# Kernel tuning notes

Hardware: AMD Instinct MI355X
Metric: run time of the kernel (lower is better)

Reference implementation:

```python
import jax, jax.numpy as jnp
import numpy as np
from jax import lax

B = 2; H = 96; W = 96
WS = 8; SHIFT = WS // 2; NW = H // WS; P = WS * WS
NH = 3; HD = 32; CD = 96; TD = 96
MID = 2 * CD; GA = 16; BASES = 16

def _rel_index():
    g = np.stack(np.meshgrid(np.arange(WS), np.arange(WS), indexing='ij'), -1).reshape(-1, 2)
    rel = g[:, None, :] - g[None, :, :] + WS - 1
    return jnp.asarray(rel[..., 0] * (2 * WS - 1) + rel[..., 1])  # [P, P]

REL_IDX = _rel_index()

def _sw_mask():
    m = np.zeros((NW, NW, WS, WS, WS, WS), bool); s = WS - SHIFT
    m[-1, :, :s, :, s:, :] = True
    m[-1, :, s:, :, :s, :] = True
    m[:, -1, :, :s, :, s:] = True
    m[:, -1, :, s:, :, :s] = True
    return jnp.asarray(m.reshape(NW * NW, P, P))

SW_MASK = _sw_mask()

def _ln(x, g, b, eps=1e-5):
    mu = x.mean(-1, keepdims=True)
    v = ((x - mu) ** 2).mean(-1, keepdims=True)
    return (x - mu) * lax.rsqrt(v + eps) * g + b

def _conv1x1(x, w):
    return jnp.einsum('bchw,oc->bohw', x, w)

def _conv3x3(x, w, b=None, groups=1):
    y = lax.conv_general_dilated(x, w, (1, 1), ((1, 1), (1, 1)),
                                 dimension_numbers=('NCHW', 'OIHW', 'NCHW'),
                                 feature_group_count=groups)
    return y if b is None else y + b[None, :, None, None]

def _unfold3(x):
    # torch F.unfold(k=3,p=1): channel-major patch order (c, kh, kw)
    bs, c, h, w = x.shape
    xp = jnp.pad(x, ((0, 0), (0, 0), (1, 1), (1, 1)))
    pats = jnp.stack([xp[:, :, i:i + h, j:j + w] for i in range(3) for j in range(3)], axis=2)
    return pats.reshape(bs, c * 9, h * w)

def _adaconv(x, ada_w, p1w, p1b, p2w, p2b):
    bs, c, h, w = x.shape
    para = jax.nn.relu(_conv1x1(x, p1w) + p1b[None, :, None, None])
    para = _conv3x3(para, p2w, p2b).reshape(bs, BASES, h * w)      # [b, r, p]
    xu = _unfold3(x).reshape(bs, GA, (c // GA) * 9, h * w)          # [b, g, d, p]
    # out[b,g,o,p] = sum_{d,r} ada_w[g,o,d,r] * xu[b,g,d,p] * para[b,r,p]
    t = jnp.einsum('godr,bgdp->bgorp', ada_w, xu)
    out = jnp.einsum('bgorp,brp->bgop', t, para)
    return out.reshape(bs, c, h, w)

def _conv_block(x, ln_g, ln_b, c1_pw, c1_dw, c2_pw, ada_w, p1w, p1b, p2w, p2b, c3_w):
    r = _ln(x.transpose(0, 2, 3, 1), ln_g, ln_b).transpose(0, 3, 1, 2)
    b1 = _conv3x3(_conv1x1(r, c1_pw), c1_dw, groups=MID)
    b2 = jax.nn.gelu(_adaconv(_conv1x1(r, c2_pw), ada_w, p1w, p1b, p2w, p2b), approximate=False)
    return x + _conv1x1(b1 * b2, c3_w)

def _wmsa(x, qkv_w, qkv_b, rel_pos, proj_w, proj_b):
    bs = x.shape[0]
    x = jnp.roll(x, (-SHIFT, -SHIFT), (1, 2))
    qkv = jnp.einsum('bhwc,oc->bhwo', x, qkv_w) + qkv_b
    qkv = qkv.reshape(bs, NW, WS, NW, WS, 3, NH, HD)
    qkv = qkv.transpose(5, 6, 0, 1, 3, 2, 4, 7).reshape(3, NH, bs, NW * NW, P, HD)
    q, k, v = qkv[0], qkv[1], qkv[2]
    sim = jnp.einsum('hbwpc,hbwqc->hbwpq', q, k) * (HD ** -0.5)
    bias = rel_pos[REL_IDX.reshape(-1)].reshape(P, P, NH).transpose(2, 0, 1)
    sim = sim + bias[:, None, None]
    sim = jnp.where(SW_MASK[None, None], -jnp.inf, sim)
    attn = jax.nn.softmax(sim, axis=-1)
    out = jnp.einsum('hbwpq,hbwqc->hbwpc', attn, v)
    out = out.reshape(NH, bs, NW, NW, WS, WS, HD).transpose(1, 2, 4, 3, 5, 0, 6).reshape(bs, H, W, NH * HD)
    out = jnp.einsum('bhwc,oc->bhwo', out, proj_w) + proj_b
    return jnp.roll(out, (SHIFT, SHIFT), (1, 2))

def _swin_block(x, ln1_g, ln1_b, qkv_w, qkv_b, rel_pos, proj_w, proj_b,
                ln2_g, ln2_b, f_w1, f_b1, f_dw, f_db, f_w2, f_b2):
    xt = x.transpose(0, 2, 3, 1)  # b h w c
    xt = xt + _wmsa(_ln(xt, ln1_g, ln1_b), qkv_w, qkv_b, rel_pos, proj_w, proj_b)
    y = _ln(xt, ln2_g, ln2_b).transpose(0, 3, 1, 2)
    y = _conv1x1(y, f_w1) + f_b1[None, :, None, None]
    y = _conv3x3(y, f_dw, f_db, groups=2 * TD)
    y = jax.nn.gelu(y, approximate=False)
    y = _conv1x1(y, f_w2) + f_b2[None, :, None, None]
    xt = xt + y.transpose(0, 2, 3, 1)
    return xt.transpose(0, 3, 1, 2)

def _block(x, cb_ln_g, cb_ln_b, cb_c1_pw, cb_c1_dw, cb_c2_pw, ada_w, ada_p1_w, ada_p1_b,
           ada_p2_w, ada_p2_b, cb_c3_w, ln1_g, ln1_b, qkv_w, qkv_b, rel_pos, proj_w, proj_b,
           ln2_g, ln2_b, ffn_w1, ffn_b1, ffn_dw, ffn_db, ffn_w2, ffn_b2, out_w, out_b):
    conv_x, trans_x = x[:, :CD], x[:, CD:]
    conv_x = _conv_block(conv_x, cb_ln_g, cb_ln_b, cb_c1_pw, cb_c1_dw, cb_c2_pw,
                         ada_w, ada_p1_w, ada_p1_b, ada_p2_w, ada_p2_b, cb_c3_w)
    trans_x = _swin_block(trans_x, ln1_g, ln1_b, qkv_w, qkv_b, rel_pos, proj_w, proj_b,
                          ln2_g, ln2_b, ffn_w1, ffn_b1, ffn_dw, ffn_db, ffn_w2, ffn_b2)
    res = _conv1x1(jnp.concatenate([conv_x, trans_x], axis=1), out_w) + out_b[None, :, None, None]
    return x + res

def setup_inputs():
    key = jax.random.key(0)
    ks = jax.random.split(key, 20)
    n = lambda i, shape, s=0.05: jax.random.normal(ks[i], shape, jnp.float32) * s
    return {
        'x': jax.random.normal(ks[0], (B, CD + TD, H, W), jnp.float32),
        'cb_ln_g': jnp.ones((CD,), jnp.float32), 'cb_ln_b': jnp.zeros((CD,), jnp.float32),
        'cb_c1_pw': n(1, (MID, CD)), 'cb_c1_dw': n(2, (MID, 1, 3, 3)),
        'cb_c2_pw': n(3, (MID, CD)),
        'ada_w': n(4, (GA, MID // GA, (MID // GA) * 9, BASES)),
        'ada_p1_w': n(5, (BASES, MID)), 'ada_p1_b': jnp.zeros((BASES,), jnp.float32),
        'ada_p2_w': n(6, (BASES, BASES, 3, 3)), 'ada_p2_b': jnp.zeros((BASES,), jnp.float32),
        'cb_c3_w': n(7, (CD, MID)),
        'ln1_g': jnp.ones((TD,), jnp.float32), 'ln1_b': jnp.zeros((TD,), jnp.float32),
        'qkv_w': n(8, (3 * TD, TD)), 'qkv_b': jnp.zeros((3 * TD,), jnp.float32),
        'rel_pos': n(9, ((2 * WS - 1) ** 2, NH), 0.02),
        'proj_w': n(10, (TD, TD)), 'proj_b': jnp.zeros((TD,), jnp.float32),
        'ln2_g': jnp.ones((TD,), jnp.float32), 'ln2_b': jnp.zeros((TD,), jnp.float32),
        'ffn_w1': n(11, (2 * TD, TD)), 'ffn_b1': jnp.zeros((2 * TD,), jnp.float32),
        'ffn_dw': n(12, (2 * TD, 1, 3, 3)), 'ffn_db': jnp.zeros((2 * TD,), jnp.float32),
        'ffn_w2': n(13, (TD, 2 * TD)), 'ffn_b2': jnp.zeros((TD,), jnp.float32),
        'out_w': n(14, (CD + TD, CD + TD)), 'out_b': jnp.zeros((CD + TD,), jnp.float32),
    }

def reference(x, cb_ln_g, cb_ln_b, cb_c1_pw, cb_c1_dw, cb_c2_pw, ada_w, ada_p1_w, ada_p1_b,
              ada_p2_w, ada_p2_b, cb_c3_w, ln1_g, ln1_b, qkv_w, qkv_b, rel_pos, proj_w, proj_b,
              ln2_g, ln2_b, ffn_w1, ffn_b1, ffn_dw, ffn_db, ffn_w2, ffn_b2, out_w, out_b):
    return _block(x, cb_ln_g, cb_ln_b, cb_c1_pw, cb_c1_dw, cb_c2_pw, ada_w, ada_p1_w, ada_p1_b,
                  ada_p2_w, ada_p2_b, cb_c3_w, ln1_g, ln1_b, qkv_w, qkv_b, rel_pos, proj_w, proj_b,
                  ln2_g, ln2_b, ffn_w1, ffn_b1, ffn_dw, ffn_db, ffn_w2, ffn_b2, out_w, out_b)
```

## Files before the change

### kernel.cpp

```cpp
#include <hip/hip_runtime.h>
#include <math.h>

#define HW_ 9216
#define IH 96
#define IW 96
#define NB 2
#define ST (NB*HW_)

typedef __attribute__((ext_vector_type(8))) short bf16x8;
typedef __attribute__((ext_vector_type(4))) float f32x4;
typedef unsigned short u16;

__device__ __forceinline__ float gelu_f(float v){
  return 0.5f*v*(1.0f+erff(v*0.70710678118654752440f));
}
__device__ __forceinline__ unsigned f2bf(float f){
  unsigned u = __float_as_uint(f);
  return (u + 0x7FFF + ((u>>16)&1)) >> 16;
}
__device__ __forceinline__ float bfl(unsigned u){ return __uint_as_float(u<<16); }
__device__ __forceinline__ float bfh(unsigned u){ return __uint_as_float(u & 0xffff0000u); }

__device__ __forceinline__ void ln12_body(const float* __restrict__ x,
    const float* __restrict__ g1, const float* __restrict__ b1,
    const float* __restrict__ g2, const float* __restrict__ b2,
    u16* __restrict__ lnc, u16* __restrict__ ln1o,
    float* __restrict__ xc, float* __restrict__ xt, int bidx)
{
  __shared__ float t[192][33];
  const int p0 = bidx<<5;
  const int bb = p0/HW_, hw0 = p0 - bb*HW_;
  const int tid = threadIdx.x;
  const int px = tid & 31, cr = tid >> 5;
  const float* xb = x + (size_t)bb*192*HW_ + hw0;
  #pragma unroll
  for (int k=0;k<24;k++){
    int c = cr + k*8;
    t[c][px] = xb[(size_t)c*HW_ + px];
  }
  __syncthreads();
  const int lane = tid&63, wv = tid>>6;
  #pragma unroll 1
  for (int i=0;i<8;i++){
    const int lp = wv*8+i;
    const size_t p = p0 + lp;
    float a0 = t[lane][lp];
    float a1 = (lane<32)? t[64+lane][lp] : 0.f;
    float c0 = t[96+lane][lp];
    float c1 = (lane<32)? t[160+lane][lp] : 0.f;
    float s1=a0+a1, s2=c0+c1;
    #pragma unroll
    for (int o=32;o;o>>=1){ s1+=__shfl_xor(s1,o); s2+=__shfl_xor(s2,o); }
    const float mu1=s1*(1.f/96.f), mu2=s2*(1.f/96.f);
    const float d0=a0-mu1, d1=a1-mu1, e0=c0-mu2, e1=c1-mu2;
    float q1=d0*d0+((lane<32)?d1*d1:0.f), q2=e0*e0+((lane<32)?e1*e1:0.f);
    #pragma unroll
    for (int o=32;o;o>>=1){ q1+=__shfl_xor(q1,o); q2+=__shfl_xor(q2,o); }
    const float r1=rsqrtf(q1*(1.f/96.f)+1e-5f), r2=rsqrtf(q2*(1.f/96.f)+1e-5f);
    lnc [p*96+lane] = (u16)f2bf(d0*r1*g1[lane]+b1[lane]);
    ln1o[p*96+lane] = (u16)f2bf(e0*r2*g2[lane]+b2[lane]);
    xc  [p*96+lane] = a0;
    xt  [p*96+lane] = c0;
    if (lane<32){
      lnc [p*96+64+lane] = (u16)f2bf(d1*r1*g1[64+lane]+b1[64+lane]);
      ln1o[p*96+64+lane] = (u16)f2bf(e1*r2*g2[64+lane]+b2[64+lane]);
      xc  [p*96+64+lane] = a1;
      xt  [p*96+64+lane] = c1;
    }
  }
}

__device__ __forceinline__ void ln_body(const float* __restrict__ in, int istride,
    const float* __restrict__ gam, const float* __restrict__ bet,
    u16* __restrict__ out, int bidx)
{
  int lane = threadIdx.x & 63;
  int wv   = threadIdx.x >> 6;
  int p    = (bidx << 2) + wv;
  const float* row = in + (size_t)p*istride;
  float v0 = row[lane];
  float v1 = (lane < 32) ? row[64+lane] : 0.0f;
  float s = v0 + v1;
  #pragma unroll
  for (int o=32;o;o>>=1) s += __shfl_xor(s,o);
  float mu = s * (1.0f/96.0f);
  float d0 = v0 - mu;
  float d1 = v1 - mu;
  float qv = d0*d0 + ((lane<32)? d1*d1 : 0.0f);
  #pragma unroll
  for (int o=32;o;o>>=1) qv += __shfl_xor(qv,o);
  float rstd = rsqrtf(qv*(1.0f/96.0f) + 1e-5f);
  u16* orow = out + (size_t)p*96;
  orow[lane] = (u16)f2bf(d0*rstd*gam[lane] + bet[lane]);
  if (lane < 32) orow[64+lane] = (u16)f2bf(d1*rstd*gam[64+lane] + bet[64+lane]);
}

template<int ACT, bool CONCAT, bool FINAL, bool HASB, bool HASR, bool OUTBF, bool SPLIT>
__device__ __forceinline__ void conv_body(unsigned char* smem,
    const u16* __restrict__ in1, const float* __restrict__ in2f, int istride,
    const u16* __restrict__ wbf, const float* __restrict__ bias,
    const float* __restrict__ res, int rstride,
    void* __restrict__ out, int ostride, int Cin, int Cout,
    u16* __restrict__ out2, int bx, int by)
{
  unsigned char* actl = smem;
  unsigned char* wl   = smem + 26624;
  const int tid=threadIdx.x, lane=tid&63, wv=tid>>6;
  const int lr=lane&15, g4=lane>>4, wm=wv>>1, wn=wv&1;
  const int p0=bx<<7, co0=by<<6;

  f32x4 acc[2][4];
  #pragma unroll
  for (int m=0;m<2;m++)
    #pragma unroll
    for (int n=0;n<4;n++) acc[m][n]=(f32x4){0.f,0.f,0.f,0.f};

  for (int kc=0; kc<Cin; kc+=96){
    {
      const int row=tid>>1, half=tid&1;
      if (!CONCAT || kc==0){
        const u16* rp = in1 + (size_t)(p0+row)*istride + (CONCAT?0:kc) + half*48;
        #pragma unroll
        for (int s=0;s<6;s++)
          *(uint4*)(actl + row*208 + (half*6+s)*16) = *(const uint4*)(rp + s*8);
      } else {
        const float* rp = in2f + (size_t)(p0+row)*96 + half*48;
        #pragma unroll
        for (int s=0;s<6;s++){
          float4 a=*(const float4*)(rp+s*8), b=*(const float4*)(rp+s*8+4);
          uint4 pk;
          pk.x=f2bf(a.x)|(f2bf(a.y)<<16);
          pk.y=f2bf(a.z)|(f2bf(a.w)<<16);
          pk.z=f2bf(b.x)|(f2bf(b.y)<<16);
          pk.w=f2bf(b.z)|(f2bf(b.w)<<16);
          *(uint4*)(actl + row*208 + (half*6+s)*16) = pk;
        }
      }
    }
    {
      const int row=tid&63, grp=tid>>6;
      const int co=co0+row;
      const u16* wr = wbf + (size_t)co*Cin + kc;
      #pragma unroll
      for (int s=0;s<3;s++){
        int sl=grp*3+s;
        uint4 v={0,0,0,0};
        if (co<Cout) v=*(const uint4*)(wr + sl*8);
        *(uint4*)(wl + row*208 + sl*16)=v;
      }
    }
    __syncthreads();
    #pragma unroll
    for (int ks=0;ks<3;ks++){
      const int sl=ks*4+g4;
      bf16x8 afr[2], bfr[4];
      #pragma unroll
      for (int m=0;m<2;m++) afr[m]=*(const bf16x8*)(wl + ((wm*2+m)*16+lr)*208 + sl*16);
      #pragma unroll
      for (int n=0;n<4;n++) bfr[n]=*(const bf16x8*)(actl + (wn*64+n*16+lr)*208 + sl*16);
      #pragma unroll
      for (int m=0;m<2;m++)
        #pragma unroll
        for (int n=0;n<4;n++)
          acc[m][n]=__builtin_amdgcn_mfma_f32_16x16x32_bf16(afr[m], bfr[n], acc[m][n],0,0,0);
    }
    __syncthreads();
  }

  if (FINAL){
    float* outf = (float*)out;
    #pragma unroll
    for (int m=0;m<2;m++){
      const int cb=co0+(wm*2+m)*16+(g4<<2);
      float4 bv = make_float4(0.f,0.f,0.f,0.f);
      if (HASB) bv = *(const float4*)(bias+cb);
      #pragma unroll
      for (int n=0;n<4;n++){
        const int p=p0+wn*64+n*16+lr;
        const int bb=p/HW_, hw=p-bb*HW_;
        const float av[4]={acc[m][n].x,acc[m][n].y,acc[m][n].z,acc[m][n].w};
        const float bvv[4]={bv.x,bv.y,bv.z,bv.w};
        #pragma unroll
        for (int j=0;j<4;j++){
          size_t oi=((size_t)bb*192+cb+j)*HW_+hw;
          outf[oi]=av[j]+bvv[j]+res[oi];
        }
      }
    }
    return;
  }
  float* lt=(float*)smem;
  #pragma unroll
  for (int m=0;m<2;m++)
    #pragma unroll
    for (int n=0;n<4;n++){
      int px=wn*64+n*16+lr;
      int c=(wm*2+m)*16+(g4<<2);
      *(f32x4*)&lt[px*68+c]=acc[m][n];
    }
  __syncthreads();
  {
    const int pr=tid>>1, half=tid&1;
    const int p=p0+pr;
    #pragma unroll
    for (int s=0;s<8;s++){
      int cl=half*32+s*4;
      int co=co0+cl;
      if (co<Cout){
        float4 v=*(float4*)&lt[pr*68+cl];
        if (SPLIT){
          if (co>=384){
            const int c2 = co-384;
            const float4 bv=*(const float4*)(bias+c2);
            v.x=fmaxf(v.x+bv.x,0.f); v.y=fmaxf(v.y+bv.y,0.f);
            v.z=fmaxf(v.z+bv.z,0.f); v.w=fmaxf(v.w+bv.w,0.f);
            uint2 pk;
            pk.x = f2bf(v.x)|(f2bf(v.y)<<16);
            pk.y = f2bf(v.z)|(f2bf(v.w)<<16);
            *(uint2*)((u16*)out + (size_t)p*16 + c2) = pk;
          } else {
            const int cc = (co<192)? co : co-192;
            const int gg = cc/12, cll = cc - gg*12;
            u16* dst = out2 + ((co<192)? (size_t)0 : (size_t)ST*192)
                     + ((size_t)gg*ST + p)*12 + cll;
            uint2 pk;
            pk.x = f2bf(v.x)|(f2bf(v.y)<<16);
            pk.y = f2bf(v.z)|(f2bf(v.w)<<16);
            *(uint2*)dst = pk;
          }
          continue;
        }
        if (HASB){ const float4 bv=*(const float4*)(bias+co); v.x+=bv.x;v.y+=bv.y;v.z+=bv.z;v.w+=bv.w; }
        if (ACT==1){
          v.x=fmaxf(v.x,0.f); v.y=fmaxf(v.y,0.f); v.z=fmaxf(v.z,0.f); v.w=fmaxf(v.w,0.f);
        }
        if (HASR){ const float4 rv=*(const float4*)(res+(size_t)p*rstride+co); v.x+=rv.x;v.y+=rv.y;v.z+=rv.z;v.w+=rv.w; }
        if (OUTBF){
          uint2 pk;
          pk.x = f2bf(v.x)|(f2bf(v.y)<<16);
          pk.y = f2bf(v.z)|(f2bf(v.w)<<16);
          *(uint2*)((u16*)out + (size_t)p*ostride + co) = pk;
        } else {
          *(float4*)((float*)out + (size_t)p*ostride + co) = v;
        }
      }
    }
  }
}

template<int ACT, bool CONCAT, bool FINAL, bool HASB, bool HASR, bool OUTBF, bool SPLIT>
__global__ __launch_bounds__(256) void conv_mfma_k(
    const u16* __restrict__ in1, const float* __restrict__ in2f, int istride,
    const u16* __restrict__ wbf, const float* __restrict__ bias,
    const float* __restrict__ res, int rstride,
    void* __restrict__ out, int ostride, int Cin, int Cout,
    u16* __restrict__ out2)
{
  __shared__ __align__(16) unsigned char smem[39936];
  conv_body<ACT,CONCAT,FINAL,HASB,HASR,OUTBF,SPLIT>(smem, in1, in2f, istride, wbf, bias,
      res, rstride, out, ostride, Cin, Cout, out2, blockIdx.x, blockIdx.y);
}

__device__ __forceinline__ void adaconv_body(unsigned char* smem,
    const u16* __restrict__ x1g, const u16* __restrict__ x2g,
    const float* __restrict__ para, const u16* __restrict__ apre,
    const float* __restrict__ dww, u16* __restrict__ outb2,
    int b, int g, int reg)
{
  unsigned char* HB2 = smem;
  unsigned char* HB1 = smem + 8640;
  float* PS = (float*)(smem + 17280);
  float* OS = (float*)(smem + 27520);
  float* WDW = (float*)(smem + 33664);

  const int tid=threadIdx.x, lane=tid&63, wv=tid>>6;
  const int lr=lane&15, g4=lane>>4;
  const int hi=(lane>>5)&1, lo16=(lane>>4)&1;
  const int rh=(reg/12)<<4, rw=(reg%12)<<3;

  bf16x8 af[3][5];
  {
    const u16* ag = apre + (size_t)g*30720;
    #pragma unroll
    for (int oo=0;oo<3;oo++){
      const int row=(wv*3+oo)*16+lr;
      #pragma unroll
      for (int ks=0;ks<5;ks++)
        af[oo][ks] = *(const bf16x8*)(ag + row*160 + ks*32 + g4*8);
    }
  }
  if (tid < 180){
    int hy = tid/10, hx = tid - hy*10;
    int gy = rh+hy-1, gx = rw+hx-1;
    uint2 a2={0,0},b2={0,0},c2={0,0}, a1={0,0},b1={0,0},c1={0,0};
    if ((unsigned)gy<IH && (unsigned)gx<IW){
      const size_t base = ((size_t)g*ST + (size_t)b*HW_ + gy*IW + gx)*12;
      const u16* s2 = x2g + base;
      a2=*(const uint2*)s2; b2=*(const uint2*)(s2+4); c2=*(const uint2*)(s2+8);
      const u16* s1 = x1g + base;
      a1=*(const uint2*)s1; b1=*(const uint2*)(s1+4); c1=*(const uint2*)(s1+8);
    }
    *(uint4*)(HB2 + tid*48)      = make_uint4(a2.x,a2.y,b2.x,b2.y);
    *(uint4*)(HB2 + tid*48 + 16) = make_uint4(c2.x,c2.y,0,0);
    *(uint4*)(HB1 + tid*48)      = make_uint4(a1.x,a1.y,b1.x,b1.y);
    *(uint4*)(HB1 + tid*48 + 16) = make_uint4(c1.x,c1.y,0,0);
  }
  if (tid < 108) WDW[tid] = dww[g*108 + tid];
  #pragma unroll
  for (int it=0; it<2; ++it){
    int idx = tid + (it<<8);
    int sub = idx >> 8;
    int p = (idx>>2)&63, q = idx&3;
    int gy = rh + (sub<<3) + (p>>3), gx = rw + (p&7);
    float4 v = *(const float4*)(para + ((size_t)b*HW_+gy*IW+gx)*16 + q*4);
    *(float4*)&PS[sub*1280 + p*20 + q*4] = v;
  }
  __syncthreads();

  int tapoff[5];
  tapoff[0] = hi ? 48   : 0;
  tapoff[1] = hi ? 480  : 96;
  tapoff[2] = hi ? 576  : 528;
  tapoff[3] = hi ? 1008 : 960;
  tapoff[4] = 1056;

  #pragma unroll
  for (int sub=0; sub<2; ++sub){
    const int sy = sub<<3;
    const int base0 = ((sy + (lr>>3))*10 + (lr&7))*48 + lo16*16;

    f32x4 acc[3][4];
    #pragma unroll
    for (int oo=0;oo<3;oo++)
      #pragma unroll
      for (int n=0;n<4;n++) acc[oo][n]=(f32x4){0.f,0.f,0.f,0.f};

    #pragma unroll
    for (int ks=0;ks<5;ks++){
      bf16x8 bfr[4];
      #pragma unroll
      for (int n=0;n<4;n++)
        bfr[n] = *(const bf16x8*)(HB2 + base0 + n*960 + tapoff[ks]);
      #pragma unroll
      for (int oo=0;oo<3;oo++)
        #pragma unroll
        for (int n=0;n<4;n++)
          acc[oo][n]=__builtin_amdgcn_mfma_f32_16x16x32_bf16(af[oo][ks], bfr[n], acc[oo][n],0,0,0);
    }

    const float* ps = &PS[sub*1280];
    #pragma unroll
    for (int oo=0;oo<3;oo++){
      const int o=wv*3+oo;
      #pragma unroll
      for (int n=0;n<4;n++){
        const int p=(n<<4)+lr;
        const f32x4 prv = *(const f32x4*)&ps[p*20+(g4<<2)];
        float s=acc[oo][n].x*prv.x+acc[oo][n].y*prv.y+acc[oo][n].z*prv.z+acc[oo][n].w*prv.w;
        s += __shfl_xor(s,16); s += __shfl_xor(s,32);
        if (g4==n) OS[((sub<<6)+p)*12+o] = gelu_f(s);
      }
    }
  }
  __syncthreads();
  {
    const size_t gb = (size_t)b*HW_;
    for (int idx=tid; idx<384; idx+=256){
      const int cq = idx % 3;
      const int rest = idx / 3;
      const int p = rest & 63, sub = rest >> 6;
      const int py = p>>3, px = p&7;
      const int Y = (sub<<3)+py, X = px;
      const unsigned char* hb1 = HB1 + (Y*10+X)*48 + cq*8;
      const float* wd = &WDW[cq*36];
      float v0=0.f,v1=0.f,v2=0.f,v3=0.f;
      #pragma unroll
      for (int i=0;i<3;i++){
        #pragma unroll
        for (int j=0;j<3;j++){
          const uint2 r = *(const uint2*)(hb1 + (i*10+j)*48);
          const int tp=i*3+j;
          v0 += bfl(r.x)*wd[tp];      v1 += bfh(r.x)*wd[9+tp];
          v2 += bfl(r.y)*wd[18+tp];   v3 += bfh(r.y)*wd[27+tp];
        }
      }
      const size_t gi = (gb + (rh+(sub<<3)+py)*IW + (rw+px))*192 + g*12 + cq*4;
      const float* os = &OS[((sub<<6)+p)*12 + cq*4];
      uint2 pk;
      pk.x = f2bf(os[0]*v0) | (f2bf(os[1]*v1)<<16);
      pk.y = f2bf(os[2]*v2) | (f2bf(os[3]*v3)<<16);
      *(uint2*)(outb2 + gi) = pk;
    }
  }
}

__device__ __forceinline__ void allprep_body(
    const float* __restrict__ s0, const float* __restrict__ s1,
    const float* __restrict__ s2, const float* __restrict__ s3,
    const float* __restrict__ s4, const float* __restrict__ s5,
    const float* __restrict__ s6, const float* __restrict__ s7,
    const float* __restrict__ p1w, const float* __restrict__ aw,
    u16* __restrict__ wdst, u16* __restrict__ apre, int bid)
{
  const int tid = threadIdx.x;
  if (bid < 648){
    const int blks[8]={108,72,72,72,36,72,72,144};
    const int off[8] ={0,27648,46080,66048,84480,93696,112128,130560};
    const int sz[8]  ={27648,18432,18432,18432,9216,18432,18432,36864};
    int m=0, acc=0;
    #pragma unroll
    for (int k=0;k<8;k++){ if (bid >= acc + blks[k]){ acc += blks[k]; m=k+1; } }
    const float* s = (m==0)?s0:(m==1)?s1:(m==2)?s2:(m==3)?s3:(m==4)?s4:(m==5)?s5:(m==6)?s6:s7;
    int i = (bid-acc)*256 + tid;
    if (i < sz[m]) wdst[off[m]+i] = (u16)f2bf(s[i]);
  } else if (bid < 654){
    int i = (bid-648)*256 + tid;
    if (i < 1536){
      int o = i/96, ci = i - o*96;
      float s = 0.f;
      for (int k=0;k<192;k++) s += p1w[o*192+k]*s2[k*96+ci];
      wdst[64512+i] = (u16)f2bf(s);
    }
  } else {
    int E = (bid-654)*256 + tid;
    int g = E / 30720, e = E - g*30720;
    int row = e / 160, kp = e - row*160;
    int tap = kp >> 4, cl = kp & 15;
    int o = row >> 4, r = row & 15;
    float v = 0.f;
    if (tap < 9 && cl < 12)
      v = aw[(((size_t)(g*12+o)*108) + cl*9 + tap)*16 + r];
    apre[(size_t)g*30720 + e] = (u16)f2bf(v);
  }
}

__global__ __launch_bounds__(256) void prep_ln12_k(
    const float* s0, const float* s1, const float* s2, const float* s3,
    const float* s4, const float* s5, const float* s6, const float* s7,
    const float* p1w, const float* aw, u16* wdst, u16* apre,
    const float* x, const float* g1, const float* b1,
    const float* g2, const float* b2,
    u16* lnc, u16* ln1o, float* xc, float* xt)
{
  const int bid = blockIdx.x;
  if (bid < 2574)
    allprep_body(s0,s1,s2,s3,s4,s5,s6,s7,p1w,aw,wdst,apre,bid);
  else
    ln12_body(x,g1,b1,g2,b2,lnc,ln1o,xc,xt,bid-2574);
}

__global__ __launch_bounds__(256) void gemm12_k(
    const u16* lnc, const u16* r6, const u16* wc12p, const float* p1b,
    const u16* wqkv, const float* qkvb, u16* pa1, u16* x1g, u16* qkv)
{
  __shared__ __align__(16) unsigned char smem[39936];
  if (blockIdx.y < 7)
    conv_body<0,false,false,false,false,true,true>(smem, lnc, nullptr, 96, wc12p, p1b,
        nullptr, 0, pa1, 16, 96, 400, x1g, blockIdx.x, blockIdx.y);
  else
    conv_body<0,false,false,true,false,true,false>(smem, r6, nullptr, 96, wqkv, qkvb,
        nullptr, 0, qkv, 288, 96, 288, nullptr, blockIdx.x, blockIdx.y-7);
}

__global__ __launch_bounds__(256) void ada_proj_k(
    const u16* x1g, const u16* x2g, const float* para, const u16* apre,
    const float* dww, u16* outb2,
    const u16* r6, const u16* wproj, const float* projb, float* xt)
{
  __shared__ __align__(16) unsigned char smem[39936];
  const int bid = blockIdx.x;
  if (bid < 2304){
    const int b = bid / 1152, rem = bid - b*1152;
    const int g = rem / 72, reg = rem - g*72;
    adaconv_body(smem, x1g, x2g, para, apre, dww, outb2, b, g, reg);
  } else {
    const int bx = bid - 2304;
    conv_body<0,false,false,true,true,false,false>(smem, r6, nullptr, 96, wproj, projb,
        xt, 96, xt, 96, 96, 96, nullptr, bx % 144, bx / 144);
  }
}

__global__ __launch_bounds__(256) void c3_ln2_k(
    const u16* b2b, const u16* wc3, const float* xc, u16* r4,
    const float* xt, const float* g2, const float* bt2, u16* r6)
{
  __shared__ __align__(16) unsigned char smem[39936];
  const int bid = blockIdx.x;
  if (bid < 288)
    conv_body<0,false,false,false,true,true,false>(smem, b2b, nullptr, 192, wc3, nullptr,
        xc, 96, r4, 96, 192, 96, nullptr, bid % 144, bid / 144);
  else
    ln_body(xt, 96, g2, bt2, r6, bid-288);
}

template<bool HASB, bool DOGELU>
__global__ __launch_bounds__(256) void dw3x3_k(const u16* __restrict__ in, int istride,
                                               const float* __restrict__ w,
                                               const float* __restrict__ bias,
                                               u16* __restrict__ out, int C){
  int t = blockIdx.x*256 + threadIdx.x;
  int cg = C >> 2;
  int p = t / cg;
  if (p >= ST) return;
  int c4 = (t - p*cg) << 2;
  int bb = p / HW_, hw = p - bb*HW_;
  int hy = hw / IW, wx = hw - hy*IW;
  float w0[9], w1[9], w2[9], w3[9];
  #pragma unroll
  for (int tp=0;tp<9;tp++){
    w0[tp]=w[(c4+0)*9+tp]; w1[tp]=w[(c4+1)*9+tp]; w2[tp]=w[(c4+2)*9+tp]; w3[tp]=w[(c4+3)*9+tp];
  }
  float ax=0.f, ay=0.f, az=0.f, aw=0.f;
  #pragma unroll
  for (int i=0;i<3;i++){
    int y = hy+i-1;
    if ((unsigned)y >= IH) continue;
    #pragma unroll
    for (int j=0;j<3;j++){
      int x2 = wx+j-1;
      if ((unsigned)x2 >= IW) continue;
      const uint2 r = *(const uint2*)(in + ((size_t)bb*HW_ + y*IW + x2)*istride + c4);
      int tp=i*3+j;
      ax += bfl(r.x)*w0[tp]; ay += bfh(r.x)*w1[tp];
      az += bfl(r.y)*w2[tp]; aw += bfh(r.y)*w3[tp];
    }
  }
  if (HASB){ ax+=bias[c4]; ay+=bias[c4+1]; az+=bias[c4+2]; aw+=bias[c4+3]; }
  if (DOGELU){ ax=gelu_f(ax); ay=gelu_f(ay); az=gelu_f(az); aw=gelu_f(aw); }
  uint2 pk;
  pk.x = f2bf(ax)|(f2bf(ay)<<16);
  pk.y = f2bf(az)|(f2bf(aw)<<16);
  *(uint2*)(out + (size_t)p*C + c4) = pk;
}

__global__ __launch_bounds__(256) void p2conv_k(const u16* __restrict__ in, const float* __restrict__ w,
                                                const float* __restrict__ bias, float* __restrict__ out){
  __shared__ float ws[2304];
  int tid = threadIdx.x;
  for (int i=tid;i<2304;i+=256) ws[i]=w[i];
  __syncthreads();
  int gidx = blockIdx.x*256 + tid;
  int p = gidx >> 2, qq = gidx & 3;
  int bb = p / HW_, hw = p - bb*HW_;
  int hy = hw / IW, wx = hw - hy*IW;
  const int cb = qq<<2;
  float a0=bias[cb], a1=bias[cb+1], a2=bias[cb+2], a3=bias[cb+3];
  #pragma unroll
  for (int i=0;i<3;i++){
    int y=hy+i-1; if ((unsigned)y>=IH) continue;
    #pragma unroll
    for (int j=0;j<3;j++){
      int x2=wx+j-1; if ((unsigned)x2>=IW) continue;
      int tap=i*3+j;
      const uint4 r = *(const uint4*)(in + ((size_t)bb*HW_ + y*IW + x2)*16);
      const uint4 r2 = *(const uint4*)(in + ((size_t)bb*HW_ + y*IW + x2)*16 + 8);
      float vv[16]={bfl(r.x),bfh(r.x),bfl(r.y),bfh(r.y),bfl(r.z),bfh(r.z),bfl(r.w),bfh(r.w),
                    bfl(r2.x),bfh(r2.x),bfl(r2.y),bfh(r2.y),bfl(r2.z),bfh(r2.z),bfl(r2.w),bfh(r2.w)};
      #pragma unroll
      for (int ci=0;ci<16;ci++){
        float v = vv[ci];
        a0 += ws[(cb+0)*144 + ci*9 + tap]*v;
        a1 += ws[(cb+1)*144 + ci*9 + tap]*v;
        a2 += ws[(cb+2)*144 + ci*9 + tap]*v;
        a3 += ws[(cb+3)*144 + ci*9 + tap]*v;
      }
    }
  }
  *(float4*)(out + (size_t)p*16 + cb) = make_float4(a0,a1,a2,a3);
}

__global__ __launch_bounds__(64) void attn_k(const u16* __restrict__ qkv,
                                             const float* __restrict__ relpos,
                                             u16* __restrict__ outa){
  __shared__ float k_s[2048];
  __shared__ float v_s[2048];
  __shared__ float rel_s[225];
  const int win = blockIdx.x, head = blockIdx.y, b = blockIdx.z;
  const int wi = win/12, wj = win%12;
  const int lane = threadIdx.x;
  for (int i=lane;i<225;i+=64) rel_s[i] = relpos[i*3+head];
  const int pi = lane>>3, pj = lane&7;
  const int hr = wi*8+pi, wr = wj*8+pj;
  const int sh = (hr+4)%96, sw = (wr+4)%96;
  const size_t pix = (size_t)b*HW_ + sh*96 + sw;
  const u16* base = qkv + pix*288;
  const float SC = 0.17677669529663687f;
  float q[32];
  #pragma unroll
  for (int i=0;i<4;i++){
    const uint4 r = *(const uint4*)(base + head*32 + i*8);
    q[i*8+0]=bfl(r.x)*SC; q[i*8+1]=bfh(r.x)*SC;
    q[i*8+2]=bfl(r.y)*SC; q[i*8+3]=bfh(r.y)*SC;
    q[i*8+4]=bfl(r.z)*SC; q[i*8+5]=bfh(r.z)*SC;
    q[i*8+6]=bfl(r.w)*SC; q[i*8+7]=bfh(r.w)*SC;
  }
  #pragma unroll
  for (int i=0;i<4;i++){
    const uint4 rk = *(const uint4*)(base + 96 + head*32 + i*8);
    const uint4 rv = *(const uint4*)(base + 192 + head*32 + i*8);
    *(float4*)&k_s[(lane<<5)+i*8]   = make_float4(bfl(rk.x),bfh(rk.x),bfl(rk.y),bfh(rk.y));
    *(float4*)&k_s[(lane<<5)+i*8+4] = make_float4(bfl(rk.z),bfh(rk.z),bfl(rk.w),bfh(rk.w));
    *(float4*)&v_s[(lane<<5)+i*8]   = make_float4(bfl(rv.x),bfh(rv.x),bfl(rv.y),bfh(rv.y));
    *(float4*)&v_s[(lane<<5)+i*8+4] = make_float4(bfl(rv.z),bfh(rv.z),bfl(rv.w),bfh(rv.w));
  }
  __syncthreads();
  const bool mi = (wi==11), mj = (wj==11);
  float sc[64];
  #pragma unroll
  for (int qq=0; qq<64; qq++){
    const float4* kr4 = (const float4*)&k_s[qq<<5];
    float s = 0.f;
    #pragma unroll
    for (int i=0;i<8;i++){
      const float4 kv = kr4[i];
      s += q[4*i]*kv.x + q[4*i+1]*kv.y + q[4*i+2]*kv.z + q[4*i+3]*kv.w;
    }
    const int qi = qq>>3, qj = qq&7;
    s += rel_s[(pi-qi+7)*15 + (pj-qj+7)];
    const bool msk = (mi && ((pi<4)!=(qi<4))) || (mj && ((pj<4)!=(qj<4)));
    sc[qq] = msk ? -1e30f : s;
  }
  float m = sc[0];
  #pragma unroll
  for (int qq=1;qq<64;qq++) m = fmaxf(m, sc[qq]);
  float sum = 0.f;
  #pragma unroll
  for (int qq=0;qq<64;qq++){ float e = __expf(sc[qq]-m); sc[qq]=e; sum+=e; }
  const float inv = 1.f/sum;
  float acc[32];
  #pragma unroll
  for (int i=0;i<32;i++) acc[i]=0.f;
  #pragma unroll
  for (int qq=0;qq<64;qq++){
    const float a = sc[qq]*inv;
    const float4* vr4 = (const float4*)&v_s[qq<<5];
    #pragma unroll
    for (int i=0;i<8;i++){
      const float4 vv = vr4[i];
      acc[4*i]+=a*vv.x; acc[4*i+1]+=a*vv.y; acc[4*i+2]+=a*vv.z; acc[4*i+3]+=a*vv.w;
    }
  }
  u16* orow = outa + pix*96 + head*32;
  #pragma unroll
  for (int i=0;i<4;i++){
    uint4 pk;
    pk.x = f2bf(acc[i*8+0])|(f2bf(acc[i*8+1])<<16);
    pk.y = f2bf(acc[i*8+2])|(f2bf(acc[i*8+3])<<16);
    pk.z = f2bf(acc[i*8+4])|(f2bf(acc[i*8+5])<<16);
    pk.w = f2bf(acc[i*8+6])|(f2bf(acc[i*8+7])<<16);
    *(uint4*)(orow + i*8) = pk;
  }
}

extern "C" void kernel_launch(void* const* d_in, const int* in_sizes, int n_in,
                              void* d_out, int out_size, void* d_ws, size_t ws_size,
                              hipStream_t stream)
{
  (void)in_sizes; (void)n_in; (void)out_size; (void)ws_size;
  const float* x        = (const float*)d_in[0];
  const float* cb_ln_g  = (const float*)d_in[1];
  const float* cb_ln_b  = (const float*)d_in[2];
  const float* cb_c1_pw = (const float*)d_in[3];
  const float* cb_c1_dw = (const float*)d_in[4];
  const float* cb_c2_pw = (const float*)d_in[5];
  const float* ada_w    = (const float*)d_in[6];
  const float* ada_p1_w = (const float*)d_in[7];
  const float* ada_p1_b = (const float*)d_in[8];
  const float* ada_p2_w = (const float*)d_in[9];
  const float* ada_p2_b = (const float*)d_in[10];
  const float* cb_c3_w  = (const float*)d_in[11];
  const float* ln1_g    = (const float*)d_in[12];
  const float* ln1_b    = (const float*)d_in[13];
  const float* qkv_w    = (const float*)d_in[14];
  const float* qkv_b    = (const float*)d_in[15];
  const float* rel_pos  = (const float*)d_in[16];
  const float* proj_w   = (const float*)d_in[17];
  const float* proj_b   = (const float*)d_in[18];
  const float* ln2_g    = (const float*)d_in[19];
  const float* ln2_b    = (const float*)d_in[20];
  const float* ffn_w1   = (const float*)d_in[21];
  const float* ffn_b1   = (const float*)d_in[22];
  const float* ffn_dw   = (const float*)d_in[23];
  const float* ffn_db   = (const float*)d_in[24];
  const float* ffn_w2   = (const float*)d_in[25];
  const float* ffn_b2   = (const float*)d_in[26];
  const float* out_w    = (const float*)d_in[27];
  const float* out_b    = (const float*)d_in[28];

  char* wsb = (char*)d_ws;
  float* XC  = (float*)wsb;
  float* U0f = (float*)(wsb + (size_t)ST*96*4);
  float* XT  = (float*)(wsb + (size_t)ST*384*4);
  float* PA2 = (float*)(wsb + (size_t)ST*480*4);
  u16* B2b  = (u16*)(wsb + (size_t)ST*496*4);
  u16* LNCb = B2b  + (size_t)ST*192;
  u16* R4b  = LNCb + (size_t)ST*96;
  u16* R6b  = R4b  + (size_t)ST*96;
  u16* PA1b = R6b  + (size_t)ST*96;
  u16* Wbf  = PA1b + (size_t)ST*16;
  u16* Apre = Wbf + 167424;
  u16* QKVb = Apre + 491520;
  u16* X1G  = (u16*)U0f;
  u16* X2G  = X1G + (size_t)ST*192;
  u16* FF1b = (u16*)U0f;
  u16* DWOb = (u16*)U0f + (size_t)ST*192;

  const u16* W_qkv  = Wbf + 0;
  const u16* W_c12p = Wbf + 27648;
  const u16* W_c3   = Wbf + 66048;
  const u16* W_proj = Wbf + 84480;
  const u16* W_ffn1 = Wbf + 93696;
  const u16* W_ffn2 = Wbf + 112128;
  const u16* W_fin  = Wbf + 130560;

  prep_ln12_k<<<3150, 256, 0, stream>>>(qkv_w, cb_c1_pw, cb_c2_pw, cb_c3_w,
                                        proj_w, ffn_w1, ffn_w2, out_w,
                                        ada_p1_w, ada_w, Wbf, Apre,
                                        x, cb_ln_g, cb_ln_b, ln1_g, ln1_b,
                                        LNCb, R6b, XC, XT);

  gemm12_k<<<dim3(144, 12), 256, 0, stream>>>(LNCb, R6b, W_c12p, ada_p1_b,
                                              W_qkv, qkv_b, PA1b, X1G, QKVb);

  attn_k<<<dim3(144, 3, NB), 64, 0, stream>>>(QKVb, rel_pos, R6b);
  p2conv_k<<<(ST*4)/256, 256, 0, stream>>>(PA1b, ada_p2_w, ada_p2_b, PA2);

  ada_proj_k<<<2592, 256, 0, stream>>>(X1G, X2G, PA2, Apre, cb_c1_dw, B2b,
                                       R6b, W_proj, proj_b, XT);

  c3_ln2_k<<<4896, 256, 0, stream>>>(B2b, W_c3, XC, R4b, XT, ln2_g, ln2_b, R6b);

  conv_mfma_k<0,false,false,true,false,true,false><<<dim3(144, 3), 256, 0, stream>>>(R6b, nullptr, 96, W_ffn1, ffn_b1, nullptr, 0, FF1b, 192, 96, 192, nullptr);
  dw3x3_k<true,true><<<(ST*48)/256, 256, 0, stream>>>(FF1b, 192, ffn_dw, ffn_db, DWOb, 192);
  conv_mfma_k<0,false,false,true,true,false,false><<<dim3(144, 2), 256, 0, stream>>>(DWOb, nullptr, 192, W_ffn2, ffn_b2, XT, 96, XT, 96, 192, 96, nullptr);

  conv_mfma_k<0,true,true,true,true,false,false><<<dim3(144, 3), 256, 0, stream>>>(R4b, XT, 96, W_fin, out_b, x, 0, (float*)d_out, 0, 192, 192, nullptr);
}
```

Before: 207.0 us.

## Fuse attention and p2conv launches; remap adaconv blocks for XCD locality

Merges the window-attention kernel and the 3x3 para conv into one 64-thread launch, with block-index dispatch. This removes a launch boundary and lets the two independent stages overlap on the GPU. The p2conv part now uses 64-thread blocks, so each block reloads the 2304-float weight table into LDS four times as often, and every block statically reserves LDS for both bodies. Adaconv block indices are also remapped so that each XCD works on a fixed pair of groups, which should improve L2 reuse of the per-group weights.

```diff
diff --git a/kernel.cpp b/kernel.cpp
--- a/kernel.cpp
+++ b/kernel.cpp
@@ -462,6 +462,138 @@
         nullptr, 0, qkv, 288, 96, 288, nullptr, blockIdx.x, blockIdx.y-7);
 }
 
+__device__ __forceinline__ void attn_body(const u16* __restrict__ qkv,
+    const float* __restrict__ relpos, u16* __restrict__ outa, int bid)
+{
+  __shared__ float k_s[2048];
+  __shared__ float v_s[2048];
+  __shared__ float rel_s[225];
+  const int win = bid % 144, head = (bid/144)%3, b = bid/432;
+  const int wi = win/12, wj = win%12;
+  const int lane = threadIdx.x;
+  for (int i=lane;i<225;i+=64) rel_s[i] = relpos[i*3+head];
+  const int pi = lane>>3, pj = lane&7;
+  const int hr = wi*8+pi, wr = wj*8+pj;
+  const int sh = (hr+4)%96, sw = (wr+4)%96;
+  const size_t pix = (size_t)b*HW_ + sh*96 + sw;
+  const u16* base = qkv + pix*288;
+  const float SC = 0.17677669529663687f;
+  float q[32];
+  #pragma unroll
+  for (int i=0;i<4;i++){
+    const uint4 r = *(const uint4*)(base + head*32 + i*8);
+    q[i*8+0]=bfl(r.x)*SC; q[i*8+1]=bfh(r.x)*SC;
+    q[i*8+2]=bfl(r.y)*SC; q[i*8+3]=bfh(r.y)*SC;
+    q[i*8+4]=bfl(r.z)*SC; q[i*8+5]=bfh(r.z)*SC;
+    q[i*8+6]=bfl(r.w)*SC; q[i*8+7]=bfh(r.w)*SC;
+  }
+  #pragma unroll
+  for (int i=0;i<4;i++){
+    const uint4 rk = *(const uint4*)(base + 96 + head*32 + i*8);
+    const uint4 rv = *(const uint4*)(base + 192 + head*32 + i*8);
+    *(float4*)&k_s[(lane<<5)+i*8]   = make_float4(bfl(rk.x),bfh(rk.x),bfl(rk.y),bfh(rk.y));
+    *(float4*)&k_s[(lane<<5)+i*8+4] = make_float4(bfl(rk.z),bfh(rk.z),bfl(rk.w),bfh(rk.w));
+    *(float4*)&v_s[(lane<<5)+i*8]   = make_float4(bfl(rv.x),bfh(rv.x),bfl(rv.y),bfh(rv.y));
+    *(float4*)&v_s[(lane<<5)+i*8+4] = make_float4(bfl(rv.z),bfh(rv.z),bfl(rv.w),bfh(rv.w));
+  }
+  __syncthreads();
+  const bool mi = (wi==11), mj = (wj==11);
+  float sc[64];
+  #pragma unroll
+  for (int qq=0; qq<64; qq++){
+    const float4* kr4 = (const float4*)&k_s[qq<<5];
+    float s = 0.f;
+    #pragma unroll
+    for (int i=0;i<8;i++){
+      const float4 kv = kr4[i];
+      s += q[4*i]*kv.x + q[4*i+1]*kv.y + q[4*i+2]*kv.z + q[4*i+3]*kv.w;
+    }
+    const int qi = qq>>3, qj = qq&7;
+    s += rel_s[(pi-qi+7)*15 + (pj-qj+7)];
+    const bool msk = (mi && ((pi<4)!=(qi<4))) || (mj && ((pj<4)!=(qj<4)));
+    sc[qq] = msk ? -1e30f : s;
+  }
+  float m = sc[0];
+  #pragma unroll
+  for (int qq=1;qq<64;qq++) m = fmaxf(m, sc[qq]);
+  float sum = 0.f;
+  #pragma unroll
+  for (int qq=0;qq<64;qq++){ float e = __expf(sc[qq]-m); sc[qq]=e; sum+=e; }
+  const float inv = 1.f/sum;
+  float acc[32];
+  #pragma unroll
+  for (int i=0;i<32;i++) acc[i]=0.f;
+  #pragma unroll
+  for (int qq=0;qq<64;qq++){
+    const float a = sc[qq]*inv;
+    const float4* vr4 = (const float4*)&v_s[qq<<5];
+    #pragma unroll
+    for (int i=0;i<8;i++){
+      const float4 vv = vr4[i];
+      acc[4*i]+=a*vv.x; acc[4*i+1]+=a*vv.y; acc[4*i+2]+=a*vv.z; acc[4*i+3]+=a*vv.w;
+    }
+  }
+  u16* orow = outa + pix*96 + head*32;
+  #pragma unroll
+  for (int i=0;i<4;i++){
+    uint4 pk;
+    pk.x = f2bf(acc[i*8+0])|(f2bf(acc[i*8+1])<<16);
+    pk.y = f2bf(acc[i*8+2])|(f2bf(acc[i*8+3])<<16);
+    pk.z = f2bf(acc[i*8+4])|(f2bf(acc[i*8+5])<<16);
+    pk.w = f2bf(acc[i*8+6])|(f2bf(acc[i*8+7])<<16);
+    *(uint4*)(orow + i*8) = pk;
+  }
+}
+
+__device__ __forceinline__ void p2conv_body(const u16* __restrict__ in,
+    const float* __restrict__ w, const float* __restrict__ bias,
+    float* __restrict__ out, int bid)
+{
+  __shared__ float ws[2304];
+  int tid = threadIdx.x;
+  for (int i=tid;i<2304;i+=64) ws[i]=w[i];
+  __syncthreads();
+  int gidx = bid*64 + tid;
+  int p = gidx >> 2, qq = gidx & 3;
+  int bb = p / HW_, hw = p - bb*HW_;
+  int hy = hw / IW, wx = hw - hy*IW;
+  const int cb = qq<<2;
+  float a0=bias[cb], a1=bias[cb+1], a2=bias[cb+2], a3=bias[cb+3];
+  #pragma unroll
+  for (int i=0;i<3;i++){
+    int y=hy+i-1; if ((unsigned)y>=IH) continue;
+    #pragma unroll
+    for (int j=0;j<3;j++){
+      int x2=wx+j-1; if ((unsigned)x2>=IW) continue;
+      int tap=i*3+j;
+      const uint4 r = *(const uint4*)(in + ((size_t)bb*HW_ + y*IW + x2)*16);
+      const uint4 r2 = *(const uint4*)(in + ((size_t)bb*HW_ + y*IW + x2)*16 + 8);
+      float vv[16]={bfl(r.x),bfh(r.x),bfl(r.y),bfh(r.y),bfl(r.z),bfh(r.z),bfl(r.w),bfh(r.w),
+                    bfl(r2.x),bfh(r2.x),bfl(r2.y),bfh(r2.y),bfl(r2.z),bfh(r2.z),bfl(r2.w),bfh(r2.w)};
+      #pragma unroll
+      for (int ci=0;ci<16;ci++){
+        float v = vv[ci];
+        a0 += ws[(cb+0)*144 + ci*9 + tap]*v;
+        a1 += ws[(cb+1)*144 + ci*9 + tap]*v;
+        a2 += ws[(cb+2)*144 + ci*9 + tap]*v;
+        a3 += ws[(cb+3)*144 + ci*9 + tap]*v;
+      }
+    }
+  }
+  *(float4*)(out + (size_t)p*16 + cb) = make_float4(a0,a1,a2,a3);
+}
+
+__global__ __launch_bounds__(64) void attn_p2_k(
+    const u16* __restrict__ qkv, const float* __restrict__ relpos,
+    u16* __restrict__ outa,
+    const u16* __restrict__ pa1, const float* __restrict__ p2w,
+    const float* __restrict__ p2b, float* __restrict__ pa2)
+{
+  const int bid = blockIdx.x;
+  if (bid < 864) attn_body(qkv, relpos, outa, bid);
+  else           p2conv_body(pa1, p2w, p2b, pa2, bid-864);
+}
+
 __global__ __launch_bounds__(256) void ada_proj_k(
     const u16* x1g, const u16* x2g, const float* para, const u16* apre,
     const float* dww, u16* outb2,
@@ -470,8 +602,10 @@
   __shared__ __align__(16) unsigned char smem[39936];
   const int bid = blockIdx.x;
   if (bid < 2304){
-    const int b = bid / 1152, rem = bid - b*1152;
-    const int g = rem / 72, reg = rem - g*72;
+    const int xcd = bid & 7, j = bid >> 3;
+    const int g = xcd + ((j & 1) << 3);
+    const int t = j >> 1;
+    const int b = t / 72, reg = t - b*72;
     adaconv_body(smem, x1g, x2g, para, apre, dww, outb2, b, g, reg);
   } else {
     const int bx = bid - 2304;
@@ -531,125 +665,6 @@
   pk.x = f2bf(ax)|(f2bf(ay)<<16);
   pk.y = f2bf(az)|(f2bf(aw)<<16);
   *(uint2*)(out + (size_t)p*C + c4) = pk;
-}
-
-__global__ __launch_bounds__(256) void p2conv_k(const u16* __restrict__ in, const float* __restrict__ w,
-                                                const float* __restrict__ bias, float* __restrict__ out){
-  __shared__ float ws[2304];
-  int tid = threadIdx.x;
-  for (int i=tid;i<2304;i+=256) ws[i]=w[i];
-  __syncthreads();
-  int gidx = blockIdx.x*256 + tid;
-  int p = gidx >> 2, qq = gidx & 3;
-  int bb = p / HW_, hw = p - bb*HW_;
-  int hy = hw / IW, wx = hw - hy*IW;
-  const int cb = qq<<2;
-  float a0=bias[cb], a1=bias[cb+1], a2=bias[cb+2], a3=bias[cb+3];
-  #pragma unroll
-  for (int i=0;i<3;i++){
-    int y=hy+i-1; if ((unsigned)y>=IH) continue;
-    #pragma unroll
-    for (int j=0;j<3;j++){
-      int x2=wx+j-1; if ((unsigned)x2>=IW) continue;
-      int tap=i*3+j;
-      const uint4 r = *(const uint4*)(in + ((size_t)bb*HW_ + y*IW + x2)*16);
-      const uint4 r2 = *(const uint4*)(in + ((size_t)bb*HW_ + y*IW + x2)*16 + 8);
-      float vv[16]={bfl(r.x),bfh(r.x),bfl(r.y),bfh(r.y),bfl(r.z),bfh(r.z),bfl(r.w),bfh(r.w),
-                    bfl(r2.x),bfh(r2.x),bfl(r2.y),bfh(r2.y),bfl(r2.z),bfh(r2.z),bfl(r2.w),bfh(r2.w)};
-      #pragma unroll
-      for (int ci=0;ci<16;ci++){
-        float v = vv[ci];
-        a0 += ws[(cb+0)*144 + ci*9 + tap]*v;
-        a1 += ws[(cb+1)*144 + ci*9 + tap]*v;
-        a2 += ws[(cb+2)*144 + ci*9 + tap]*v;
-        a3 += ws[(cb+3)*144 + ci*9 + tap]*v;
-      }
-    }
-  }
-  *(float4*)(out + (size_t)p*16 + cb) = make_float4(a0,a1,a2,a3);
-}
-
-__global__ __launch_bounds__(64) void attn_k(const u16* __restrict__ qkv,
-                                             const float* __restrict__ relpos,
-                                             u16* __restrict__ outa){
-  __shared__ float k_s[2048];
-  __shared__ float v_s[2048];
-  __shared__ float rel_s[225];
-  const int win = blockIdx.x, head = blockIdx.y, b = blockIdx.z;
-  const int wi = win/12, wj = win%12;
-  const int lane = threadIdx.x;
-  for (int i=lane;i<225;i+=64) rel_s[i] = relpos[i*3+head];
-  const int pi = lane>>3, pj = lane&7;
-  const int hr = wi*8+pi, wr = wj*8+pj;
-  const int sh = (hr+4)%96, sw = (wr+4)%96;
-  const size_t pix = (size_t)b*HW_ + sh*96 + sw;
-  const u16* base = qkv + pix*288;
-  const float SC = 0.17677669529663687f;
-  float q[32];
-  #pragma unroll
-  for (int i=0;i<4;i++){
-    const uint4 r = *(const uint4*)(base + head*32 + i*8);
-    q[i*8+0]=bfl(r.x)*SC; q[i*8+1]=bfh(r.x)*SC;
-    q[i*8+2]=bfl(r.y)*SC; q[i*8+3]=bfh(r.y)*SC;
-    q[i*8+4]=bfl(r.z)*SC; q[i*8+5]=bfh(r.z)*SC;
-    q[i*8+6]=bfl(r.w)*SC; q[i*8+7]=bfh(r.w)*SC;
-  }
-  #pragma unroll
-  for (int i=0;i<4;i++){
-    const uint4 rk = *(const uint4*)(base + 96 + head*32 + i*8);
-    const uint4 rv = *(const uint4*)(base + 192 + head*32 + i*8);
-    *(float4*)&k_s[(lane<<5)+i*8]   = make_float4(bfl(rk.x),bfh(rk.x),bfl(rk.y),bfh(rk.y));
-    *(float4*)&k_s[(lane<<5)+i*8+4] = make_float4(bfl(rk.z),bfh(rk.z),bfl(rk.w),bfh(rk.w));
-    *(float4*)&v_s[(lane<<5)+i*8]   = make_float4(bfl(rv.x),bfh(rv.x),bfl(rv.y),bfh(rv.y));
-    *(float4*)&v_s[(lane<<5)+i*8+4] = make_float4(bfl(rv.z),bfh(rv.z),bfl(rv.w),bfh(rv.w));
-  }
-  __syncthreads();
-  const bool mi = (wi==11), mj = (wj==11);
-  float sc[64];
-  #pragma unroll
-  for (int qq=0; qq<64; qq++){
-    const float4* kr4 = (const float4*)&k_s[qq<<5];
-    float s = 0.f;
-    #pragma unroll
-    for (int i=0;i<8;i++){
-      const float4 kv = kr4[i];
-      s += q[4*i]*kv.x + q[4*i+1]*kv.y + q[4*i+2]*kv.z + q[4*i+3]*kv.w;
-    }
-    const int qi = qq>>3, qj = qq&7;
-    s += rel_s[(pi-qi+7)*15 + (pj-qj+7)];
-    const bool msk = (mi && ((pi<4)!=(qi<4))) || (mj && ((pj<4)!=(qj<4)));
-    sc[qq] = msk ? -1e30f : s;
-  }
-  float m = sc[0];
-  #pragma unroll
-  for (int qq=1;qq<64;qq++) m = fmaxf(m, sc[qq]);
-  float sum = 0.f;
-  #pragma unroll
-  for (int qq=0;qq<64;qq++){ float e = __expf(sc[qq]-m); sc[qq]=e; sum+=e; }
-  const float inv = 1.f/sum;
-  float acc[32];
-  #pragma unroll
-  for (int i=0;i<32;i++) acc[i]=0.f;
-  #pragma unroll
-  for (int qq=0;qq<64;qq++){
-    const float a = sc[qq]*inv;
-    const float4* vr4 = (const float4*)&v_s[qq<<5];
-    #pragma unroll
-    for (int i=0;i<8;i++){
-      const float4 vv = vr4[i];
-      acc[4*i]+=a*vv.x; acc[4*i+1]+=a*vv.y; acc[4*i+2]+=a*vv.z; acc[4*i+3]+=a*vv.w;
-    }
-  }
-  u16* orow = outa + pix*96 + head*32;
-  #pragma unroll
-  for (int i=0;i<4;i++){
-    uint4 pk;
-    pk.x = f2bf(acc[i*8+0])|(f2bf(acc[i*8+1])<<16);
-    pk.y = f2bf(acc[i*8+2])|(f2bf(acc[i*8+3])<<16);
-    pk.z = f2bf(acc[i*8+4])|(f2bf(acc[i*8+5])<<16);
-    pk.w = f2bf(acc[i*8+6])|(f2bf(acc[i*8+7])<<16);
-    *(uint4*)(orow + i*8) = pk;
-  }
 }
 
 extern "C" void kernel_launch(void* const* d_in, const int* in_sizes, int n_in,
@@ -722,8 +737,8 @@
   gemm12_k<<<dim3(144, 12), 256, 0, stream>>>(LNCb, R6b, W_c12p, ada_p1_b,
                                               W_qkv, qkv_b, PA1b, X1G, QKVb);
 
-  attn_k<<<dim3(144, 3, NB), 64, 0, stream>>>(QKVb, rel_pos, R6b);
-  p2conv_k<<<(ST*4)/256, 256, 0, stream>>>(PA1b, ada_p2_w, ada_p2_b, PA2);
+  attn_p2_k<<<2016, 64, 0, stream>>>(QKVb, rel_pos, R6b,
+                                     PA1b, ada_p2_w, ada_p2_b, PA2);
 
   ada_proj_k<<<2592, 256, 0, stream>>>(X1G, X2G, PA2, Apre, cb_c1_dw, B2b,
                                        R6b, W_proj, proj_b, XT);
```

Result: faster. 191.7 us (-7.4%).
